# Optimization experiments

Measured on AMD Instinct MI355X. Metric: run time of the kernel, lower is better.

The kernel has to match this reference:

```python
import jax, jax.numpy as jnp
import numpy as np

EMBED_DIM = 1024
NUM_HEADS = 16
HEAD_DIM = EMBED_DIM // NUM_HEADS
SEG_LENS = [1024, 2048, 4096]
DIL_RATIOS = [1, 2, 4]
NEG = -1e8  # lse fill value used by sparse_to_dense


def setup_inputs() -> dict:
    root = jax.random.key(0)
    ks = jax.random.split(root, 12)
    B, L, E = 1, 4096, EMBED_DIM
    s = 0.02
    return {
        "query": jax.random.normal(ks[0], (B, L, E), jnp.float32),
        "key": jax.random.normal(ks[1], (B, L, E), jnp.float32),
        "value": jax.random.normal(ks[2], (B, L, E), jnp.float32),
        "Wq": jax.random.normal(ks[3], (E, E), jnp.float32) * s,
        "bq": jnp.zeros((E,), jnp.float32),
        "Wk": jax.random.normal(ks[4], (E, E), jnp.float32) * s,
        "bk": jnp.zeros((E,), jnp.float32),
        "Wv": jax.random.normal(ks[5], (E, E), jnp.float32) * s,
        "bv": jnp.zeros((E,), jnp.float32),
        "Wo": jax.random.normal(ks[6], (E, E), jnp.float32) * s,
        "bo": jnp.zeros((E,), jnp.float32),
    }


def _branch(q, k, v, sl, dr, L):
    """One (segment_length, dilated_ratio) branch.
    q,k,v: (B, L, H, D). Returns dense out (B, H, L, D) and lse (B, H, L).
    """
    B = q.shape[0]
    H, D = NUM_HEADS, HEAD_DIM
    sl = min(sl, L)
    pad = (-L) % sl
    if pad:
        pw = ((0, 0), (0, pad), (0, 0), (0, 0))
        q, k, v = jnp.pad(q, pw), jnp.pad(k, pw), jnp.pad(v, pw)
    n = (L + pad) // sl  # segments
    qs = q.reshape(B * n, sl, H, D)
    ks = k.reshape(B * n, sl, H, D)
    vs = v.reshape(B * n, sl, H, D)
    # dense_to_sparse: head j (group r = j // (H//dr)) keeps positions i*dr + r
    hg = H // dr
    g = sl // dr
    grp = jnp.arange(H) // hg                      # (H,)
    pos = jnp.arange(g)[:, None] * dr + grp[None]  # (g, H) dense positions
    hidx = jnp.arange(H)[None, :]
    sp = lambda x: x[:, pos, hidx, :]              # (B*n, g, H, D)
    qd, kd, vd = sp(qs), sp(ks), sp(vs)
    # causal attention within each sparse segment (flash_attn semantics)
    scores = jnp.einsum('bqhd,bkhd->bhqk', qd, kd) * (D ** -0.5)
    mask = jnp.tril(jnp.ones((g, g), bool))
    scores = jnp.where(mask, scores, -jnp.inf)
    lse = jax.nn.logsumexp(scores, axis=-1)        # (B*n, H, g)
    o = jnp.einsum('bhqk,bkhd->bqhd', jnp.exp(scores - lse[..., None]), vd)
    # sparse_to_dense: scatter back onto dense positions, NEG elsewhere
    hcol = jnp.arange(H)[:, None]                  # (H,1)
    od = jnp.zeros((B * n, H, sl, D), o.dtype).at[:, hcol, pos.T].set(
        o.transpose(0, 2, 1, 3))
    ld = jnp.zeros((B * n, H, sl), lse.dtype).at[:, hcol, pos.T].set(lse)
    ld = jnp.where(ld == 0.0, NEG, ld)  # matches masked_fill_(lse == 0, -1e8)
    od = od.reshape(B, n, H, sl, D).transpose(0, 2, 1, 3, 4)
    od = od.reshape(B, H, n * sl, D)[:, :, :L]
    ld = ld.reshape(B, n, H, sl).transpose(0, 2, 1, 3).reshape(B, H, n * sl)[:, :, :L]
    return od, ld


def reference(query, key, value, Wq, bq, Wk, bk, Wv, bv, Wo, bo):
    B, L, E = query.shape
    H, D = NUM_HEADS, HEAD_DIM
    q = (query @ Wq.T + bq).reshape(B, L, H, D)
    k = (key @ Wk.T + bk).reshape(B, L, H, D)
    v = (value @ Wv.T + bv).reshape(B, L, H, D)
    outs, lses = [], []
    for sl, dr in zip(SEG_LENS, DIL_RATIOS):
        o, l = _branch(q, k, v, sl, dr, L)
        outs.append(o)
        lses.append(l)
    lse_all = jnp.stack(lses, 0)[..., None]        # (nb, B, H, L, 1)
    m = lse_all.max(0)
    w = jnp.exp(lse_all - m)
    w = w / w.sum(0)                               # softmax merge weights
    w = jax.lax.stop_gradient(w)                   # torch computes under no_grad
    out = sum(o * wi.astype(o.dtype) for o, wi in zip(outs, w))  # (B,H,L,D)
    out = out.transpose(0, 2, 1, 3).reshape(B, L, E)
    return out @ Wo.T + bo
```

## Files before the change

kernel.cpp:

```cpp
#include <hip/hip_runtime.h>
#include <math.h>


#define L_SEQ 4096
#define EDIM  1024
#define NH    16
#define HD    64
#define GLEN  1024

typedef __bf16 bf16;
typedef __bf16 bf16x8 __attribute__((ext_vector_type(8)));
typedef __bf16 bf16x4 __attribute__((ext_vector_type(4)));
typedef short  s16x4  __attribute__((ext_vector_type(4)));
typedef float  f32x4  __attribute__((ext_vector_type(4)));

template <bool B> struct Flag { static constexpr bool v = B; };

__device__ __forceinline__ void gload16(const bf16* g, bf16* l) {
  __builtin_amdgcn_global_load_lds(
      (__attribute__((address_space(1))) void*)(const_cast<bf16*>(g)),
      (__attribute__((address_space(3))) void*)(l),
      16, 0, 0);
}

__device__ __forceinline__ f32x4 mfma16x16x16_bf16(bf16x4 a, bf16x4 b, f32x4 c) {
#if defined(__HIP_DEVICE_COMPILE__)
  union { bf16x4 h; s16x4 s; } ua, ub;
  ua.h = a; ub.h = b;
  return __builtin_amdgcn_mfma_f32_16x16x16bf16_1k(ua.s, ub.s, c, 0, 0, 0);
#else
  (void)a; (void)b;
  return c;
#endif
}

__device__ __forceinline__ float fast_exp2(float x) {
#if __has_builtin(__builtin_amdgcn_exp2f)
  return __builtin_amdgcn_exp2f(x);
#else
  return __expf(x * 0.6931471805599453f);
#endif
}

__global__ __launch_bounds__(256) void cvt_kernel(
    const float* q, const float* k, const float* v,
    const float* wq, const float* wk, const float* wv, const float* wo,
    bf16* oq, bf16* ok, bf16* ov,
    bf16* owq, bf16* owk, bf16* owv, bf16* owo)
{
  const float* src; bf16* dst; int n;
  switch (blockIdx.y) {
    case 0: src = q;  dst = oq;  n = L_SEQ*EDIM; break;
    case 1: src = k;  dst = ok;  n = L_SEQ*EDIM; break;
    case 2: src = v;  dst = ov;  n = L_SEQ*EDIM; break;
    case 3: src = wq; dst = owq; n = EDIM*EDIM; break;
    case 4: src = wk; dst = owk; n = EDIM*EDIM; break;
    case 5: src = wv; dst = owv; n = EDIM*EDIM; break;
    default: src = wo; dst = owo; n = EDIM*EDIM; break;
  }
  int i = (blockIdx.x * 256 + threadIdx.x) * 8;
  if (i >= n) return;
  const float4* s4 = (const float4*)(src + i);
  float4 a = s4[0], b = s4[1];
  bf16x8 o = { (bf16)a.x, (bf16)a.y, (bf16)a.z, (bf16)a.w,
               (bf16)b.x, (bf16)b.y, (bf16)b.z, (bf16)b.w };
  *(bf16x8*)(dst + i) = o;
}

template <typename OutT>
__device__ __forceinline__ void gemm_body(const bf16* __restrict__ A,
                                          const bf16* __restrict__ W,
                                          const float* __restrict__ bias,
                                          OutT* __restrict__ C)
{
  constexpr int K = 1024;
  __shared__ __align__(16) bf16 lA[128 * 32];
  __shared__ __align__(16) bf16 lB[128 * 32];

  const int tid  = threadIdx.x;
  const int lane = tid & 63;
  const int w    = tid >> 6;
  const int quad = lane >> 4;
  const int l16  = lane & 15;
  const int wr   = w >> 1, wc = w & 1;
  const int row0 = blockIdx.y * 128;
  const int col0 = blockIdx.x * 128;

  f32x4 acc[4][4] = {};

  const int c0 = tid, c1 = tid + 256;
  const bf16* Ab0 = A + (size_t)(row0 + (c0 >> 2)) * K + (c0 & 3) * 8;
  const bf16* Ab1 = A + (size_t)(row0 + (c1 >> 2)) * K + (c1 & 3) * 8;
  const bf16* Bb0 = W + (size_t)(col0 + (c0 >> 2)) * K + (c0 & 3) * 8;
  const bf16* Bb1 = W + (size_t)(col0 + (c1 >> 2)) * K + (c1 & 3) * 8;
  bf16* lA0 = &lA[c0 * 8]; bf16* lA1 = &lA[c1 * 8];
  bf16* lB0 = &lB[c0 * 8]; bf16* lB1 = &lB[c1 * 8];

  for (int kt = 0; kt < K; kt += 32) {
    __syncthreads();
    gload16(Ab0 + kt, lA0);
    gload16(Ab1 + kt, lA1);
    gload16(Bb0 + kt, lB0);
    gload16(Bb1 + kt, lB1);
    __syncthreads();

    bf16x8 af[4], bfrag[4];
#pragma unroll
    for (int mi = 0; mi < 4; mi++)
      af[mi] = *(const bf16x8*)&lA[(wr * 64 + mi * 16 + l16) * 32 + quad * 8];
#pragma unroll
    for (int ni = 0; ni < 4; ni++)
      bfrag[ni] = *(const bf16x8*)&lB[(wc * 64 + ni * 16 + l16) * 32 + quad * 8];
#pragma unroll
    for (int mi = 0; mi < 4; mi++)
#pragma unroll
      for (int ni = 0; ni < 4; ni++)
        acc[mi][ni] = __builtin_amdgcn_mfma_f32_16x16x32_bf16(
            af[mi], bfrag[ni], acc[mi][ni], 0, 0, 0);
  }

#pragma unroll
  for (int mi = 0; mi < 4; mi++) {
#pragma unroll
    for (int ni = 0; ni < 4; ni++) {
      const int gcol = col0 + wc * 64 + ni * 16 + l16;
      const float bv = bias[gcol];
#pragma unroll
      for (int r = 0; r < 4; r++) {
        const int grow = row0 + wr * 64 + mi * 16 + quad * 4 + r;
        C[(size_t)grow * 1024 + gcol] = (OutT)(acc[mi][ni][r] + bv);
      }
    }
  }
}

__global__ __launch_bounds__(256) void gemm_qkv_kernel(
    const bf16* xq, const bf16* xk, const bf16* xv,
    const bf16* wq, const bf16* wk, const bf16* wv,
    const float* bq, const float* bk, const float* bv,
    bf16* q, bf16* k, bf16* v)
{
  const bf16 *A, *W; const float* bias; bf16* C;
  if (blockIdx.z == 0)      { A = xq; W = wq; bias = bq; C = q; }
  else if (blockIdx.z == 1) { A = xk; W = wk; bias = bk; C = k; }
  else                      { A = xv; W = wv; bias = bv; C = v; }
  gemm_body<bf16>(A, W, bias, C);
}

__global__ __launch_bounds__(256) void gemm_out_kernel(
    const bf16* A, const bf16* W, const float* bias, float* C)
{
  gemm_body<float>(A, W, bias, C);
}

__global__ __launch_bounds__(256) void vtrans_kernel(
    const bf16* __restrict__ v, bf16* vt0, bf16* vt1, bf16* vt2)
{
  __shared__ __align__(16) bf16 ltile[64 * 72];
  const int bid = blockIdx.x;
  int sl, dr, rem, shift; bf16* vt;
  if (bid < 1024)      { sl = 1024; dr = 1; rem = bid;        vt = vt0; shift = 4; }
  else if (bid < 1536) { sl = 2048; dr = 2; rem = bid - 1024; vt = vt1; shift = 3; }
  else                 { sl = 4096; dr = 4; rem = bid - 1536; vt = vt2; shift = 2; }
  const int ktile = rem & 15;
  const int h     = (rem >> 4) & 15;
  const int seg   = rem >> 8;
  const int grp   = h >> shift;
  const int segbase = seg * sl;
  const int tid = threadIdx.x;
  {
    const int i = tid >> 2, dc = tid & 3;
    const size_t p = (size_t)(segbase + (ktile * 64 + i) * dr + grp);
    const bf16* src = v + p * EDIM + h * 64 + dc * 16;
    *(uint4*)&ltile[i * 72 + dc * 16]     = *(const uint4*)(src);
    *(uint4*)&ltile[i * 72 + dc * 16 + 8] = *(const uint4*)(src + 8);
  }
  __syncthreads();
  {
    const int d = tid >> 2, kc = tid & 3;
    __align__(16) bf16 tmp[16];
#pragma unroll
    for (int j = 0; j < 16; j++) tmp[j] = ltile[(kc * 16 + j) * 72 + d];
    bf16* dst = vt + ((size_t)(seg * NH + h) * 64 + d) * GLEN + ktile * 64 + kc * 16;
    *(uint4*)dst       = *(uint4*)&tmp[0];
    *(uint4*)(dst + 8) = *(uint4*)&tmp[8];
  }
}

__global__ __launch_bounds__(256, 4) void attn_kernel(
    const bf16* __restrict__ qg, const bf16* __restrict__ kg,
    const bf16* vt0, const bf16* vt1, const bf16* vt2,
    bf16* o0, bf16* o1, bf16* o2,
    float* l0, float* l1, float* l2)
{
  __shared__ __align__(16) bf16 lK[2][64 * 64];
  __shared__ __align__(16) bf16 lV[2][64 * 64];

  const int bid0 = blockIdx.x;
  const int o = (bid0 & 7) * 112 + (bid0 >> 3);

  int sl, dr, rem, shift;
  const bf16* vt; bf16* ob; float* lseb;
  if (o < 512)      { sl = 1024; dr = 1; rem = o;       vt = vt0; ob = o0; lseb = l0; shift = 4; }
  else if (o < 768) { sl = 2048; dr = 2; rem = o - 512; vt = vt1; ob = o1; lseb = l1; shift = 3; }
  else              { sl = 4096; dr = 4; rem = o - 768; vt = vt2; ob = o2; lseb = l2; shift = 2; }
  const int j   = rem & 7;
  const int h   = (rem >> 3) & 15;
  const int seg = rem >> 7;
  const int qtA = 15 - j;
  const int qtB = j;
  const int grp = h >> shift;
  const int segbase = seg * sl;

  const int tid = threadIdx.x, lane = tid & 63, w = tid >> 6;
  const int quad = lane >> 4, l16 = lane & 15;
  const int rs8 = l16 & 7;

  auto loadq = [&](int qt, bf16x8& a0, bf16x8& a1) {
    const int qi = qt * 64 + w * 16 + l16;
    const size_t p = (size_t)(segbase + qi * dr + grp);
    const bf16* qp = qg + p * EDIM + h * 64 + quad * 8;
    a0 = *(const bf16x8*)(qp);
    a1 = *(const bf16x8*)(qp + 32);
  };
  bf16x8 qaA0, qaA1, qaB0, qaB1;
  loadq(qtA, qaA0, qaA1);
  loadq(qtB, qaB0, qaB1);

  f32x4 OA[4] = {}, OB[4] = {};
  float mA = -__builtin_inff(), lA_ = 0.f;
  float mB = -__builtin_inff(), lB_ = 0.f;

  const bf16* vbase = vt + (size_t)(seg * NH + h) * 64 * GLEN;
  const int c0 = tid, c1 = tid + 256;
  const int r0 = c0 >> 3, sw0 = ((c0 & 7) ^ (r0 & 7));
  const int r1 = c1 >> 3, sw1 = ((c1 & 7) ^ (r1 & 7));

  const bf16* kp0 = kg + (size_t)(segbase + r0 * dr + grp) * EDIM + h * 64 + sw0 * 8;
  const bf16* kp1 = kg + (size_t)(segbase + r1 * dr + grp) * EDIM + h * 64 + sw1 * 8;
  const bf16* vp0 = vbase + (size_t)r0 * GLEN + sw0 * 8;
  const bf16* vp1 = vbase + (size_t)r1 * GLEN + sw1 * 8;
  const size_t kstep = (size_t)64 * dr * EDIM;

  auto stage = [&](int buf) {
    gload16(kp0, &lK[buf][c0 * 8]);
    gload16(kp1, &lK[buf][c1 * 8]);
    gload16(vp0, &lV[buf][c0 * 8]);
    gload16(vp1, &lV[buf][c1 * 8]);
    kp0 += kstep; kp1 += kstep; vp0 += 64; vp1 += 64;
  };

  const float CS = 0.18033688011112042f;
  const int qiA = qtA * 64 + w * 16 + l16;
  const int qiB = qtB * 64 + w * 16 + l16;

  const int kb0 = l16 * 64 + ((quad ^ rs8) * 8);
  const int kb1 = l16 * 64 + (((4 + quad) ^ rs8) * 8);
  const int vb0 = l16 * 64 + (quad & 1) * 4;

  auto comp = [&](auto hasB_, auto diagA_, auto diagB_, int kt) {
    constexpr bool HAS_B  = decltype(hasB_)::v;
    constexpr bool DIAG_A = decltype(diagA_)::v;
    constexpr bool DIAG_B = decltype(diagB_)::v;
    const bf16* bK = lK[kt & 1];
    const bf16* bV = lV[kt & 1];

    f32x4 sA[4], sB[4];
#pragma unroll
    for (int t = 0; t < 4; t++) {
      const bool aA = !DIAG_A || t <= w;
      const bool aB = HAS_B && (!DIAG_B || t <= w);
      if (aA || aB) {
        bf16x8 ka0 = *(const bf16x8*)&bK[kb0 + t * 1024];
        bf16x8 ka1 = *(const bf16x8*)&bK[kb1 + t * 1024];
        if (aA) {
          sA[t] = f32x4{0.f, 0.f, 0.f, 0.f};
          sA[t] = __builtin_amdgcn_mfma_f32_16x16x32_bf16(ka0, qaA0, sA[t], 0, 0, 0);
          sA[t] = __builtin_amdgcn_mfma_f32_16x16x32_bf16(ka1, qaA1, sA[t], 0, 0, 0);
        }
        if (aB) {
          sB[t] = f32x4{0.f, 0.f, 0.f, 0.f};
          sB[t] = __builtin_amdgcn_mfma_f32_16x16x32_bf16(ka0, qaB0, sB[t], 0, 0, 0);
          sB[t] = __builtin_amdgcn_mfma_f32_16x16x32_bf16(ka1, qaB1, sB[t], 0, 0, 0);
        }
      }
    }

    float mrA = -__builtin_inff(), mrB = -__builtin_inff();
#pragma unroll
    for (int t = 0; t < 4; t++) {
      if (!DIAG_A || t <= w) {
#pragma unroll
        for (int r = 0; r < 4; r++) {
          float sv = sA[t][r];
          if (DIAG_A) {
            const int kj = kt * 64 + t * 16 + quad * 4 + r;
            if (kj > qiA) sv = -__builtin_inff();
          }
          sA[t][r] = sv;
          mrA = fmaxf(mrA, sv);
        }
      }
      if (HAS_B && (!DIAG_B || t <= w)) {
#pragma unroll
        for (int r = 0; r < 4; r++) {
          float sv = sB[t][r];
          if (DIAG_B) {
            const int kj = kt * 64 + t * 16 + quad * 4 + r;
            if (kj > qiB) sv = -__builtin_inff();
          }
          sB[t][r] = sv;
          mrB = fmaxf(mrB, sv);
        }
      }
    }
    mrA = fmaxf(mrA, __shfl_xor(mrA, 16, 64));
    mrA = fmaxf(mrA, __shfl_xor(mrA, 32, 64));
    if constexpr (HAS_B) {
      mrB = fmaxf(mrB, __shfl_xor(mrB, 16, 64));
      mrB = fmaxf(mrB, __shfl_xor(mrB, 32, 64));
    }

    {
      const float mnew = fmaxf(mA, mrA * CS);
      if (!__all(mnew - mA <= 8.0f)) {
        const float alpha = fast_exp2(mA - mnew);
#pragma unroll
        for (int nf = 0; nf < 4; nf++)
#pragma unroll
          for (int r = 0; r < 4; r++) OA[nf][r] *= alpha;
        lA_ *= alpha;
        mA = mnew;
      }
    }
    if constexpr (HAS_B) {
      const float mnew = fmaxf(mB, mrB * CS);
      if (!__all(mnew - mB <= 8.0f)) {
        const float alpha = fast_exp2(mB - mnew);
#pragma unroll
        for (int nf = 0; nf < 4; nf++)
#pragma unroll
          for (int r = 0; r < 4; r++) OB[nf][r] *= alpha;
        lB_ *= alpha;
        mB = mnew;
      }
    }

    bf16x4 pbA[4], pbB[4];
    float rsA = 0.f, rsB = 0.f;
#pragma unroll
    for (int t = 0; t < 4; t++) {
      if (!DIAG_A || t <= w) {
#pragma unroll
        for (int r = 0; r < 4; r++) {
          const float pv = fast_exp2(__builtin_fmaf(sA[t][r], CS, -mA));
          pbA[t][r] = (bf16)pv;
          rsA += pv;
        }
      }
      if (HAS_B && (!DIAG_B || t <= w)) {
#pragma unroll
        for (int r = 0; r < 4; r++) {
          const float pv = fast_exp2(__builtin_fmaf(sB[t][r], CS, -mB));
          pbB[t][r] = (bf16)pv;
          rsB += pv;
        }
      }
    }
    rsA += __shfl_xor(rsA, 16, 64);
    rsA += __shfl_xor(rsA, 32, 64);
    lA_ += rsA;
    if constexpr (HAS_B) {
      rsB += __shfl_xor(rsB, 16, 64);
      rsB += __shfl_xor(rsB, 32, 64);
      lB_ += rsB;
    }

#pragma unroll
    for (int t = 0; t < 4; t++) {
      const bool aA = !DIAG_A || t <= w;
      const bool aB = HAS_B && (!DIAG_B || t <= w);
      if (aA || aB) {
        const int cx = (((2 * t) + (quad >> 1)) ^ rs8) * 8;
#pragma unroll
        for (int nf = 0; nf < 4; nf++) {
          bf16x4 va = *(const bf16x4*)&bV[vb0 + nf * 1024 + cx];
          if (aA) OA[nf] = mfma16x16x16_bf16(va, pbA[t], OA[nf]);
          if (aB) OB[nf] = mfma16x16x16_bf16(va, pbB[t], OB[nf]);
        }
      }
    }
  };

  stage(0);
  int kt = 0;
  for (; kt < qtB; kt++) {
    __syncthreads();
    stage((kt + 1) & 1);
    comp(Flag<true>{}, Flag<false>{}, Flag<false>{}, kt);
  }
  __syncthreads();
  stage((kt + 1) & 1);
  comp(Flag<true>{}, Flag<false>{}, Flag<true>{}, kt);
  kt++;
  for (; kt < qtA; kt++) {
    __syncthreads();
    stage((kt + 1) & 1);
    comp(Flag<false>{}, Flag<false>{}, Flag<false>{}, kt);
  }
  __syncthreads();
  comp(Flag<false>{}, Flag<true>{}, Flag<false>{}, kt);

  auto epilogue = [&](const f32x4 (&Oa)[4], float m_r, float l_r, int qt) {
    const int qi = qt * 64 + w * 16 + l16;
    const float linv = 1.0f / l_r;
    const int pdense = segbase + qi * dr + grp;
    bf16* orow = ob + (size_t)pdense * EDIM + h * 64;
#pragma unroll
    for (int nf = 0; nf < 4; nf++) {
      bf16x4 ov;
#pragma unroll
      for (int r = 0; r < 4; r++) ov[r] = (bf16)(Oa[nf][r] * linv);
      *(bf16x4*)(orow + nf * 16 + quad * 4) = ov;
    }
    if (quad == 0)
      lseb[h * L_SEQ + pdense] = m_r * 0.6931471805599453f + __logf(l_r);
  };
  epilogue(OA, mA, lA_, qtA);
  epilogue(OB, mB, lB_, qtB);
}

__global__ __launch_bounds__(256) void merge_kernel(
    const bf16* __restrict__ o0, const bf16* __restrict__ o1, const bf16* __restrict__ o2,
    const float* __restrict__ l0, const float* __restrict__ l1, const float* __restrict__ l2,
    bf16* __restrict__ merged)
{
  const int idx = blockIdx.x * 256 + threadIdx.x;
  const int dc = idx & 7;
  const int h  = (idx >> 3) & 15;
  const int p  = idx >> 7;
  const bool c1 = ((p & 1) == (h >> 3));
  const bool c2 = ((p & 3) == (h >> 2));
  const float s0 = l0[h * L_SEQ + p];
  const float s1 = c1 ? l1[h * L_SEQ + p] : -__builtin_inff();
  const float s2 = c2 ? l2[h * L_SEQ + p] : -__builtin_inff();
  const float mx = fmaxf(s0, fmaxf(s1, s2));
  float w0 = __expf(s0 - mx);
  float w1 = c1 ? __expf(s1 - mx) : 0.f;
  float w2 = c2 ? __expf(s2 - mx) : 0.f;
  const float inv = 1.0f / (w0 + w1 + w2);
  w0 *= inv; w1 *= inv; w2 *= inv;

  const size_t off = (size_t)p * EDIM + h * 64 + dc * 8;
  float acc[8];
  bf16x8 a0 = *(const bf16x8*)(o0 + off);
#pragma unroll
  for (int j = 0; j < 8; j++) acc[j] = w0 * (float)a0[j];
  if (c1) {
    bf16x8 a1 = *(const bf16x8*)(o1 + off);
#pragma unroll
    for (int j = 0; j < 8; j++) acc[j] += w1 * (float)a1[j];
  }
  if (c2) {
    bf16x8 a2 = *(const bf16x8*)(o2 + off);
#pragma unroll
    for (int j = 0; j < 8; j++) acc[j] += w2 * (float)a2[j];
  }
  bf16x8 r;
#pragma unroll
  for (int j = 0; j < 8; j++) r[j] = (bf16)acc[j];
  *(bf16x8*)(merged + off) = r;
}

extern "C" void kernel_launch(void* const* d_in, const int* in_sizes, int n_in,
                              void* d_out, int out_size, void* d_ws, size_t ws_size,
                              hipStream_t stream)
{
  (void)in_sizes; (void)n_in; (void)out_size; (void)ws_size;
  const float* query = (const float*)d_in[0];
  const float* key   = (const float*)d_in[1];
  const float* value = (const float*)d_in[2];
  const float* Wq = (const float*)d_in[3];
  const float* bq = (const float*)d_in[4];
  const float* Wk = (const float*)d_in[5];
  const float* bk = (const float*)d_in[6];
  const float* Wv = (const float*)d_in[7];
  const float* bv = (const float*)d_in[8];
  const float* Wo = (const float*)d_in[9];
  const float* bo = (const float*)d_in[10];

  char* base = (char*)d_ws;
  size_t off = 0;
  auto take = [&](size_t nbytes) -> char* {
    char* p = base + off;
    off += (nbytes + 255) & ~(size_t)255;
    return p;
  };
  const size_t LE2 = (size_t)L_SEQ * EDIM * 2;
  const size_t EE2 = (size_t)EDIM * EDIM * 2;
  bf16* xq  = (bf16*)take(LE2);
  bf16* xk  = (bf16*)take(LE2);
  bf16* xv  = (bf16*)take(LE2);
  bf16* wqb = (bf16*)take(EE2);
  bf16* wkb = (bf16*)take(EE2);
  bf16* wvb = (bf16*)take(EE2);
  bf16* wob = (bf16*)take(EE2);
  bf16* qb  = (bf16*)take(LE2);
  bf16* kb  = (bf16*)take(LE2);
  bf16* vb  = (bf16*)take(LE2);
  bf16* vt0 = (bf16*)take((size_t)4 * NH * HD * GLEN * 2);
  bf16* vt1 = (bf16*)take((size_t)2 * NH * HD * GLEN * 2);
  bf16* vt2 = (bf16*)take((size_t)1 * NH * HD * GLEN * 2);
  float* lse0 = (float*)take((size_t)NH * L_SEQ * 4);
  float* lse1 = (float*)take((size_t)NH * L_SEQ * 4);
  float* lse2 = (float*)take((size_t)NH * L_SEQ * 4);
  bf16* merged = (bf16*)take(LE2);
  bf16* o0 = xq; bf16* o1 = xk; bf16* o2 = xv;

  dim3 blk(256);
  cvt_kernel<<<dim3(2048, 7), blk, 0, stream>>>(
      query, key, value, Wq, Wk, Wv, Wo, xq, xk, xv, wqb, wkb, wvb, wob);
  gemm_qkv_kernel<<<dim3(8, 32, 3), blk, 0, stream>>>(
      xq, xk, xv, wqb, wkb, wvb, bq, bk, bv, qb, kb, vb);
  vtrans_kernel<<<dim3(1792), blk, 0, stream>>>(vb, vt0, vt1, vt2);
  attn_kernel<<<dim3(896), blk, 0, stream>>>(
      qb, kb, vt0, vt1, vt2, o0, o1, o2, lse0, lse1, lse2);
  merge_kernel<<<dim3(2048), blk, 0, stream>>>(
      o0, o1, o2, lse0, lse1, lse2, merged);
  gemm_out_kernel<<<dim3(8, 32), blk, 0, stream>>>(merged, wob, bo, (float*)d_out);
}
```

Before: 228.8 us.

## Interleave V-transpose layout for 128-bit LDS reads, add setprio and vector reductions

Changes the transposed V layout so that each lane can load 8 bf16 values in one 128-bit LDS read and split them across two adjacent key tiles' MFMAs, replacing two 64-bit reads. It also remaps GEMM block indices to group row tiles for better L2 reuse. It wraps the MFMA sections in s_setprio, and splits the max and sum reductions into per-register vector accumulators to shorten dependency chains. The layout change must match exactly between the transpose writer and the attention reader, and the GEMM remap assumes a specific grid shape.

```diff
diff --git a/kernel.cpp b/kernel.cpp
--- a/kernel.cpp
+++ b/kernel.cpp
@@ -83,8 +83,10 @@
   const int quad = lane >> 4;
   const int l16  = lane & 15;
   const int wr   = w >> 1, wc = w & 1;
-  const int row0 = blockIdx.y * 128;
-  const int col0 = blockIdx.x * 128;
+  const int ly = blockIdx.x * 4 + (blockIdx.y >> 3);
+  const int lx = blockIdx.y & 7;
+  const int row0 = ly * 128;
+  const int col0 = lx * 128;
 
   f32x4 acc[4][4] = {};
 
@@ -181,9 +183,15 @@
     __align__(16) bf16 tmp[16];
 #pragma unroll
     for (int j = 0; j < 16; j++) tmp[j] = ltile[(kc * 16 + j) * 72 + d];
-    bf16* dst = vt + ((size_t)(seg * NH + h) * 64 + d) * GLEN + ktile * 64 + kc * 16;
-    *(uint4*)dst       = *(uint4*)&tmp[0];
-    *(uint4*)(dst + 8) = *(uint4*)&tmp[8];
+    const int p2 = kc >> 1, half = kc & 1;
+    bf16* dst = vt + ((size_t)(seg * NH + h) * 64 + d) * GLEN + ktile * 64
+                   + p2 * 32 + half * 4;
+#pragma unroll
+    for (int q = 0; q < 4; q++) {
+      bf16x4 piece = { tmp[q * 4 + 0], tmp[q * 4 + 1],
+                       tmp[q * 4 + 2], tmp[q * 4 + 3] };
+      *(bf16x4*)(dst + q * 8) = piece;
+    }
   }
 }
 
@@ -251,12 +259,13 @@
   };
 
   const float CS = 0.18033688011112042f;
+  const float NEGINF = -__builtin_inff();
   const int qiA = qtA * 64 + w * 16 + l16;
   const int qiB = qtB * 64 + w * 16 + l16;
 
   const int kb0 = l16 * 64 + ((quad ^ rs8) * 8);
   const int kb1 = l16 * 64 + (((4 + quad) ^ rs8) * 8);
-  const int vb0 = l16 * 64 + (quad & 1) * 4;
+  const int vb0 = l16 * 64;
 
   auto comp = [&](auto hasB_, auto diagA_, auto diagB_, int kt) {
     constexpr bool HAS_B  = decltype(hasB_)::v;
@@ -266,6 +275,7 @@
     const bf16* bV = lV[kt & 1];
 
     f32x4 sA[4], sB[4];
+    __builtin_amdgcn_s_setprio(1);
 #pragma unroll
     for (int t = 0; t < 4; t++) {
       const bool aA = !DIAG_A || t <= w;
@@ -285,8 +295,10 @@
         }
       }
     }
-
-    float mrA = -__builtin_inff(), mrB = -__builtin_inff();
+    __builtin_amdgcn_s_setprio(0);
+
+    f32x4 mvA = {NEGINF, NEGINF, NEGINF, NEGINF};
+    f32x4 mvB = {NEGINF, NEGINF, NEGINF, NEGINF};
 #pragma unroll
     for (int t = 0; t < 4; t++) {
       if (!DIAG_A || t <= w) {
@@ -295,10 +307,10 @@
           float sv = sA[t][r];
           if (DIAG_A) {
             const int kj = kt * 64 + t * 16 + quad * 4 + r;
-            if (kj > qiA) sv = -__builtin_inff();
+            if (kj > qiA) sv = NEGINF;
           }
           sA[t][r] = sv;
-          mrA = fmaxf(mrA, sv);
+          mvA[r] = fmaxf(mvA[r], sv);
         }
       }
       if (HAS_B && (!DIAG_B || t <= w)) {
@@ -307,13 +319,15 @@
           float sv = sB[t][r];
           if (DIAG_B) {
             const int kj = kt * 64 + t * 16 + quad * 4 + r;
-            if (kj > qiB) sv = -__builtin_inff();
+            if (kj > qiB) sv = NEGINF;
           }
           sB[t][r] = sv;
-          mrB = fmaxf(mrB, sv);
-        }
-      }
-    }
+          mvB[r] = fmaxf(mvB[r], sv);
+        }
+      }
+    }
+    float mrA = fmaxf(fmaxf(mvA[0], mvA[1]), fmaxf(mvA[2], mvA[3]));
+    float mrB = fmaxf(fmaxf(mvB[0], mvB[1]), fmaxf(mvB[2], mvB[3]));
     mrA = fmaxf(mrA, __shfl_xor(mrA, 16, 64));
     mrA = fmaxf(mrA, __shfl_xor(mrA, 32, 64));
     if constexpr (HAS_B) {
@@ -347,7 +361,7 @@
     }
 
     bf16x4 pbA[4], pbB[4];
-    float rsA = 0.f, rsB = 0.f;
+    f32x4 rvA = {0.f, 0.f, 0.f, 0.f}, rvB = {0.f, 0.f, 0.f, 0.f};
 #pragma unroll
     for (int t = 0; t < 4; t++) {
       if (!DIAG_A || t <= w) {
@@ -355,7 +369,7 @@
         for (int r = 0; r < 4; r++) {
           const float pv = fast_exp2(__builtin_fmaf(sA[t][r], CS, -mA));
           pbA[t][r] = (bf16)pv;
-          rsA += pv;
+          rvA[r] += pv;
         }
       }
       if (HAS_B && (!DIAG_B || t <= w)) {
@@ -363,33 +377,44 @@
         for (int r = 0; r < 4; r++) {
           const float pv = fast_exp2(__builtin_fmaf(sB[t][r], CS, -mB));
           pbB[t][r] = (bf16)pv;
-          rsB += pv;
-        }
-      }
-    }
+          rvB[r] += pv;
+        }
+      }
+    }
+    float rsA = (rvA[0] + rvA[1]) + (rvA[2] + rvA[3]);
     rsA += __shfl_xor(rsA, 16, 64);
     rsA += __shfl_xor(rsA, 32, 64);
     lA_ += rsA;
     if constexpr (HAS_B) {
+      float rsB = (rvB[0] + rvB[1]) + (rvB[2] + rvB[3]);
       rsB += __shfl_xor(rsB, 16, 64);
       rsB += __shfl_xor(rsB, 32, 64);
       lB_ += rsB;
     }
 
-#pragma unroll
-    for (int t = 0; t < 4; t++) {
-      const bool aA = !DIAG_A || t <= w;
-      const bool aB = HAS_B && (!DIAG_B || t <= w);
-      if (aA || aB) {
-        const int cx = (((2 * t) + (quad >> 1)) ^ rs8) * 8;
+    __builtin_amdgcn_s_setprio(1);
+#pragma unroll
+    for (int p2 = 0; p2 < 2; p2++) {
+      const int t0 = 2 * p2, t1 = t0 + 1;
+      const bool aA0 = !DIAG_A || t0 <= w;
+      const bool aA1 = !DIAG_A || t1 <= w;
+      const bool aB0 = HAS_B && (!DIAG_B || t0 <= w);
+      const bool aB1 = HAS_B && (!DIAG_B || t1 <= w);
+      if (aA0 || aA1 || aB0 || aB1) {
+        const int cx = ((p2 * 4 + quad) ^ rs8) * 8;
 #pragma unroll
         for (int nf = 0; nf < 4; nf++) {
-          bf16x4 va = *(const bf16x4*)&bV[vb0 + nf * 1024 + cx];
-          if (aA) OA[nf] = mfma16x16x16_bf16(va, pbA[t], OA[nf]);
-          if (aB) OB[nf] = mfma16x16x16_bf16(va, pbB[t], OB[nf]);
-        }
-      }
-    }
+          bf16x8 va8 = *(const bf16x8*)&bV[vb0 + nf * 1024 + cx];
+          bf16x4 vlo = __builtin_shufflevector(va8, va8, 0, 1, 2, 3);
+          bf16x4 vhi = __builtin_shufflevector(va8, va8, 4, 5, 6, 7);
+          if (aA0) OA[nf] = mfma16x16x16_bf16(vlo, pbA[t0], OA[nf]);
+          if (aA1) OA[nf] = mfma16x16x16_bf16(vhi, pbA[t1], OA[nf]);
+          if (aB0) OB[nf] = mfma16x16x16_bf16(vlo, pbB[t0], OB[nf]);
+          if (aB1) OB[nf] = mfma16x16x16_bf16(vhi, pbB[t1], OB[nf]);
+        }
+      }
+    }
+    __builtin_amdgcn_s_setprio(0);
   };
 
   stage(0);
```

Measured after the change: 227.2 us. About the same (-0.7%).
